# Kernel tuning notes

Hardware: AMD Instinct MI355X
Metric: run time of the kernel (lower is better)

Reference implementation:

```python
import jax, jax.numpy as jnp
import numpy as np
import math

EPS = 1e-5
MAX_NORM = 1.0 - 1e-3
C = 1.0
NUM_HEADS = 8


def _project(x, c=C):
    norm = jnp.maximum(jnp.linalg.norm(x, axis=-1, keepdims=True), EPS)
    max_norm = MAX_NORM / math.sqrt(c)
    return jnp.where(norm > max_norm, x / norm * max_norm, x)


def _expmap0(v, c=C):
    sc = math.sqrt(c)
    n = jnp.maximum(jnp.linalg.norm(v, axis=-1, keepdims=True), EPS)
    return _project(jnp.tanh(sc * n) * v / (sc * n), c)


def _logmap0(y, c=C):
    sc = math.sqrt(c)
    n = jnp.maximum(jnp.linalg.norm(y, axis=-1, keepdims=True), EPS)
    return jnp.arctanh(jnp.minimum(sc * n, 1.0 - EPS)) * y / (sc * n)


def _mobius_add(x, y, c=C):
    x2 = jnp.sum(x * x, axis=-1, keepdims=True)
    y2 = jnp.sum(y * y, axis=-1, keepdims=True)
    xy = jnp.sum(x * y, axis=-1, keepdims=True)
    num = (1.0 + 2.0 * c * xy + c * y2) * x + (1.0 - c * x2) * y
    den = jnp.maximum(1.0 + 2.0 * c * xy + c * c * x2 * y2, EPS)
    return _project(num / den, c)


def _pairwise_dist(x, y, c=C):
    # x: (B,H,Q,d), y: (B,H,K,d) -> (B,H,Q,K)
    m = _mobius_add(-x[:, :, :, None, :], y[:, :, None, :, :], c)  # (B,H,Q,K,d)
    n = jnp.clip(jnp.linalg.norm(m, axis=-1), EPS, 1.0 - EPS)
    sc = math.sqrt(c)
    return (2.0 / sc) * jnp.arctanh(sc * n)


def setup_inputs() -> dict:
    key = jax.random.key(0)
    ks = jax.random.split(key, 12)
    B, S, D = 2, 512, 512
    # points on the Poincare ball via expmap0
    q = _expmap0(0.5 * jax.random.normal(ks[0], (B, S, D), jnp.float32))
    k = _expmap0(0.5 * jax.random.normal(ks[1], (B, S, D), jnp.float32))
    v = _expmap0(0.5 * jax.random.normal(ks[2], (B, S, D), jnp.float32))
    w = 0.02
    return {
        'query': q, 'key': k, 'value': v,
        'Wq': w * jax.random.normal(ks[3], (D, D), jnp.float32),
        'bq': w * jax.random.normal(ks[4], (D,), jnp.float32),
        'Wk': w * jax.random.normal(ks[5], (D, D), jnp.float32),
        'bk': w * jax.random.normal(ks[6], (D,), jnp.float32),
        'Wv': w * jax.random.normal(ks[7], (D, D), jnp.float32),
        'bv': w * jax.random.normal(ks[8], (D,), jnp.float32),
        'Wo': w * jax.random.normal(ks[9], (D, D), jnp.float32),
        'bo': w * jax.random.normal(ks[10], (D,), jnp.float32),
    }


def reference(query, key, value, Wq, bq, Wk, bk, Wv, bv, Wo, bo):
    B, Q, D = query.shape
    K = key.shape[1]
    H = NUM_HEADS
    dh = D // H
    q_tan = _logmap0(query)
    k_tan = _logmap0(key)
    v_tan = _logmap0(value)
    q = (q_tan @ Wq.T + bq).reshape(B, Q, H, dh).transpose(0, 2, 1, 3)  # (B,H,Q,dh)
    k = (k_tan @ Wk.T + bk).reshape(B, K, H, dh).transpose(0, 2, 1, 3)
    v = (v_tan @ Wv.T + bv).reshape(B, K, H, dh).transpose(0, 2, 1, 3)
    q_hyp = _expmap0(q)
    k_hyp = _expmap0(k)
    scores = -_pairwise_dist(q_hyp, k_hyp) / math.sqrt(dh)  # (B,H,Q,K)
    attn = jax.nn.softmax(scores, axis=-1)  # dropout is identity in eval
    out = jnp.einsum('bhqk,bhkd->bhqd', attn, v)
    out = out.transpose(0, 2, 1, 3).reshape(B, Q, D)
    return _expmap0(out @ Wo.T + bo)
```

## Files before the change

### kernel.cpp

```cpp
#include <hip/hip_runtime.h>
#include <cmath>

#define DEV static __device__ __forceinline__

namespace {

constexpr int B = 2, S = 512, D = 512, H = 8;
constexpr int BS = B * S;
constexpr float EPSF = 1e-5f;
constexpr float MAXN = 1.0f - 1e-3f;
constexpr int NSPLIT = 4;

typedef unsigned short u16;
typedef unsigned int u32;
typedef __attribute__((ext_vector_type(8))) short bf8_t;
typedef __attribute__((ext_vector_type(8))) _Float16 h8_t;
typedef __attribute__((ext_vector_type(4))) float f4_t;

DEV float waveSum(float v) {
#pragma unroll
  for (int o = 32; o > 0; o >>= 1) v += __shfl_xor(v, o, 64);
  return v;
}
DEV u16 f2bf(float f) {
  u32 x = __float_as_uint(f);
  u32 r = x + 0x7fffu + ((x >> 16) & 1u);
  return (u16)(r >> 16);
}
DEV float bf2f(u16 u) { return __uint_as_float(((u32)u) << 16); }
DEV u16 f2h(float f) {
  _Float16 h = (_Float16)f;
  u16 u;
  __builtin_memcpy(&u, &h, 2);
  return u;
}
DEV float tanh_pos(float n) {
  float e = __builtin_amdgcn_exp2f(2.8853900817779268f * n);
  return (e - 1.f) / (e + 1.f);
}
DEV bf8_t conv8(float4 a, float4 b) {
  bf8_t o;
  o[0] = (short)f2bf(a.x); o[1] = (short)f2bf(a.y);
  o[2] = (short)f2bf(a.z); o[3] = (short)f2bf(a.w);
  o[4] = (short)f2bf(b.x); o[5] = (short)f2bf(b.y);
  o[6] = (short)f2bf(b.z); o[7] = (short)f2bf(b.w);
  return o;
}
DEV float dot4(float4 a) { return a.x * a.x + a.y * a.y + a.z * a.z + a.w * a.w; }

__global__ __launch_bounds__(256) void gemm_qkv_f2(
    const float* __restrict__ q, const float* __restrict__ k,
    const float* __restrict__ v, const float* __restrict__ Wq,
    const float* __restrict__ Wk, const float* __restrict__ Wv,
    const float* __restrict__ bq, const float* __restrict__ bk,
    const float* __restrict__ bv, u16* __restrict__ hq, u16* __restrict__ hk,
    u16* __restrict__ vT, float* __restrict__ qn2, float* __restrict__ kn2) {
  const int z = blockIdx.z;
  const float* A = z == 0 ? q : (z == 1 ? k : v);
  const float* W = z == 0 ? Wq : (z == 1 ? Wk : Wv);
  const float* bias = z == 0 ? bq : (z == 1 ? bk : bv);
  const int i0 = blockIdx.y * 64, j0 = blockIdx.x * 64, h = blockIdx.x;
  __shared__ __align__(16) u16 As[4096], Bs[4096];
  __shared__ float facs[64];
  const int tid = threadIdx.x;
  const int w = tid >> 6, l = tid & 63, lg = l >> 4, lr = l & 15;
  const int srow = tid >> 3, scb = tid & 7;
  f4_t acc[4] = {{0, 0, 0, 0}, {0, 0, 0, 0}, {0, 0, 0, 0}, {0, 0, 0, 0}};
  float n2a = 0.f, n2b = 0.f;
  for (int kt = 0; kt < D; kt += 64) {
    const float* ap0 = A + (size_t)(i0 + srow) * D + kt + scb * 8;
    const float* ap1 = ap0 + (size_t)32 * D;
    const float* wp0 = W + (size_t)(j0 + srow) * D + kt + scb * 8;
    const float* wp1 = wp0 + (size_t)32 * D;
    float4 a00 = *(const float4*)ap0, a01 = *(const float4*)(ap0 + 4);
    float4 a10 = *(const float4*)ap1, a11 = *(const float4*)(ap1 + 4);
    float4 w00 = *(const float4*)wp0, w01 = *(const float4*)(wp0 + 4);
    float4 w10 = *(const float4*)wp1, w11 = *(const float4*)(wp1 + 4);
    n2a += dot4(a00) + dot4(a01);
    n2b += dot4(a10) + dot4(a11);
    __syncthreads();
    const int sw = 8 * (scb ^ (srow & 7));
    *(bf8_t*)&As[srow * 64 + sw] = conv8(a00, a01);
    *(bf8_t*)&As[(srow + 32) * 64 + sw] = conv8(a10, a11);
    *(bf8_t*)&Bs[srow * 64 + sw] = conv8(w00, w01);
    *(bf8_t*)&Bs[(srow + 32) * 64 + sw] = conv8(w10, w11);
    __syncthreads();
#pragma unroll
    for (int ks = 0; ks < 2; ++ks) {
      const int arow = w * 16 + lr;
      bf8_t af = *(const bf8_t*)&As[arow * 64 + 8 * ((ks * 4 + lg) ^ (arow & 7))];
#pragma unroll
      for (int nf = 0; nf < 4; ++nf) {
        const int brow = nf * 16 + lr;
        bf8_t bfr = *(const bf8_t*)&Bs[brow * 64 + 8 * ((ks * 4 + lg) ^ (brow & 7))];
        acc[nf] = __builtin_amdgcn_mfma_f32_16x16x32_bf16(af, bfr, acc[nf], 0, 0, 0);
      }
    }
  }
  n2a += __shfl_xor(n2a, 1, 64); n2a += __shfl_xor(n2a, 2, 64);
  n2a += __shfl_xor(n2a, 4, 64);
  n2b += __shfl_xor(n2b, 1, 64); n2b += __shfl_xor(n2b, 2, 64);
  n2b += __shfl_xor(n2b, 4, 64);
  if (scb == 0) {
    float na = fmaxf(sqrtf(n2a), EPSF), za = fminf(na, 1.0f - EPSF);
    facs[srow] = 0.34657359027997264f *
                 __builtin_amdgcn_logf((1.0f + za) / (1.0f - za)) / na;
    float nb = fmaxf(sqrtf(n2b), EPSF), zb = fminf(nb, 1.0f - EPSF);
    facs[srow + 32] = 0.34657359027997264f *
                      __builtin_amdgcn_logf((1.0f + zb) / (1.0f - zb)) / nb;
  }
  __syncthreads();
  float c[4][4];
#pragma unroll
  for (int nf = 0; nf < 4; ++nf) {
    const float bb = bias[j0 + nf * 16 + lr];
#pragma unroll
    for (int r = 0; r < 4; ++r)
      c[nf][r] = acc[nf][r] * facs[w * 16 + lg * 4 + r] + bb;
  }
  if (z < 2) {
    float part[4] = {0, 0, 0, 0};
#pragma unroll
    for (int nf = 0; nf < 4; ++nf)
#pragma unroll
      for (int r = 0; r < 4; ++r) part[r] += c[nf][r] * c[nf][r];
#pragma unroll
    for (int off = 1; off < 16; off <<= 1)
#pragma unroll
      for (int r = 0; r < 4; ++r) part[r] += __shfl_xor(part[r], off, 64);
    float fac[4];
#pragma unroll
    for (int r = 0; r < 4; ++r) {
      float n = fmaxf(sqrtf(part[r]), EPSF);
      fac[r] = fminf(tanh_pos(n), MAXN) / n;
    }
    u16 yb[4][4];
    float p2[4] = {0, 0, 0, 0};
#pragma unroll
    for (int nf = 0; nf < 4; ++nf)
#pragma unroll
      for (int r = 0; r < 4; ++r) {
        u16 t = f2bf(c[nf][r] * fac[r]);
        yb[nf][r] = t;
        float yf = bf2f(t);
        p2[r] += yf * yf;
      }
#pragma unroll
    for (int off = 1; off < 16; off <<= 1)
#pragma unroll
      for (int r = 0; r < 4; ++r) p2[r] += __shfl_xor(p2[r], off, 64);
    u16* dst = z == 0 ? hq : hk;
    float* n2o = z == 0 ? qn2 : kn2;
#pragma unroll
    for (int nf = 0; nf < 4; ++nf)
#pragma unroll
      for (int r = 0; r < 4; ++r)
        dst[(size_t)(i0 + w * 16 + lg * 4 + r) * D + j0 + nf * 16 + lr] = yb[nf][r];
    if (lr == 0)
#pragma unroll
      for (int r = 0; r < 4; ++r)
        n2o[h * BS + i0 + w * 16 + lg * 4 + r] = p2[r];
  } else {
    __syncthreads();
#pragma unroll
    for (int nf = 0; nf < 4; ++nf)
#pragma unroll
      for (int r = 0; r < 4; ++r) {
        const int prow = w * 16 + lg * 4 + r;
        const int pcol = nf * 16 + lr;
        As[prow * 64 + 8 * ((pcol >> 3) ^ (prow & 7)) + (pcol & 7)] = f2h(c[nf][r]);
      }
    __syncthreads();
    const int d = tid >> 2, s0 = (tid & 3) * 16;
    const int b = i0 >> 9, sb = (i0 & 511) + s0;
    bf8_t o0, o1;
#pragma unroll
    for (int j = 0; j < 8; ++j) {
      const int s = s0 + j;
      o0[j] = (short)As[s * 64 + 8 * ((d >> 3) ^ (s & 7)) + (d & 7)];
    }
#pragma unroll
    for (int j = 0; j < 8; ++j) {
      const int s = s0 + 8 + j;
      o1[j] = (short)As[s * 64 + 8 * ((d >> 3) ^ (s & 7)) + (d & 7)];
    }
    u16* dst = vT + ((size_t)((b * 8 + h) * 64 + d)) * S + sb;
    *(bf8_t*)dst = o0;
    *(bf8_t*)(dst + 8) = o1;
  }
}

__global__ __launch_bounds__(64) void fused_attn_sk(
    const u16* __restrict__ hq, const u16* __restrict__ hk,
    const u16* __restrict__ vT, const float* __restrict__ qn2,
    const float* __restrict__ kn2, float* __restrict__ Opart,
    float* __restrict__ rpart) {
  const int bh = blockIdx.z, b = bh >> 3, h = bh & 7;
  const int i0 = blockIdx.x * 16;
  const int sp = blockIdx.y;
  __shared__ __align__(16) u16 Ps[2][16 * 64];
  const int l = threadIdx.x, lg = l >> 4, lr = l & 15;
  bf8_t qf[2];
#pragma unroll
  for (int ks = 0; ks < 2; ++ks)
    qf[ks] = *(const bf8_t*)(hq + (size_t)(b * S + i0 + lr) * D + h * 64 +
                             ks * 32 + lg * 8);
  float qq[4];
#pragma unroll
  for (int r = 0; r < 4; ++r) qq[r] = qn2[h * BS + b * S + i0 + lg * 4 + r];
  f4_t acc_o[4] = {{0, 0, 0, 0}, {0, 0, 0, 0}, {0, 0, 0, 0}, {0, 0, 0, 0}};
  float rsum[4] = {0, 0, 0, 0};
#pragma unroll
  for (int t = 0; t < 2; ++t) {
    const int kt = sp * 2 + t;
    const int kb = b * S + kt * 64;
    bf8_t kf[2][4], vf[2][4];
#pragma unroll
    for (int ks = 0; ks < 2; ++ks)
#pragma unroll
      for (int nf = 0; nf < 4; ++nf) {
        kf[ks][nf] = *(const bf8_t*)(hk + (size_t)(kb + nf * 16 + lr) * D +
                                     h * 64 + ks * 32 + lg * 8);
        vf[ks][nf] = *(const bf8_t*)(vT + (size_t)(bh * 64 + nf * 16 + lr) * S +
                                     kt * 64 + ks * 32 + lg * 8);
      }
    float kn[4];
#pragma unroll
    for (int nf = 0; nf < 4; ++nf) kn[nf] = kn2[h * BS + kb + nf * 16 + lr];
    f4_t sa[4] = {{0, 0, 0, 0}, {0, 0, 0, 0}, {0, 0, 0, 0}, {0, 0, 0, 0}};
#pragma unroll
    for (int ks = 0; ks < 2; ++ks)
#pragma unroll
      for (int nf = 0; nf < 4; ++nf)
        sa[nf] = __builtin_amdgcn_mfma_f32_16x16x32_bf16(qf[ks], kf[ks][nf],
                                                         sa[nf], 0, 0, 0);
    u16* Pb = Ps[t & 1];
    float ps[4] = {0, 0, 0, 0};
#pragma unroll
    for (int nf = 0; nf < 4; ++nf) {
      const float kk = kn[nf];
#pragma unroll
      for (int r = 0; r < 4; ++r) {
        const float tt = sa[nf][r];
        float num = fmaxf(qq[r] - 2.f * tt + kk, 0.f);
        float den = fmaxf(1.f - 2.f * tt + qq[r] * kk, EPSF);
        float rr = fminf(fmaxf(sqrtf(num / den), EPSF), MAXN);
        float p = __builtin_amdgcn_exp2f(
            0.125f * __builtin_amdgcn_logf((1.f - rr) / (1.f + rr)));
        ps[r] += p;
        const int prow = lg * 4 + r, pcol = nf * 16 + lr;
        Pb[prow * 64 + 8 * ((pcol >> 3) ^ (prow & 7)) + (pcol & 7)] = f2h(p);
      }
    }
#pragma unroll
    for (int off = 1; off < 16; off <<= 1)
#pragma unroll
      for (int r = 0; r < 4; ++r) ps[r] += __shfl_xor(ps[r], off, 64);
#pragma unroll
    for (int r = 0; r < 4; ++r) rsum[r] += ps[r];
#pragma unroll
    for (int ks = 0; ks < 2; ++ks) {
      h8_t pa = *(const h8_t*)&Pb[lr * 64 + 8 * ((ks * 4 + lg) ^ (lr & 7))];
#pragma unroll
      for (int nf = 0; nf < 4; ++nf)
        acc_o[nf] = __builtin_amdgcn_mfma_f32_16x16x32_f16(pa, vf[ks][nf],
                                                           acc_o[nf], 0, 0, 0);
    }
  }
  float* Ob = Opart + ((size_t)(sp * 16 + bh) * S + i0) * 64;
#pragma unroll
  for (int nf = 0; nf < 4; ++nf)
#pragma unroll
    for (int r = 0; r < 4; ++r)
      Ob[(lg * 4 + r) * 64 + nf * 16 + lr] = acc_o[nf][r];
  if (lr == 0)
#pragma unroll
    for (int r = 0; r < 4; ++r)
      rpart[(size_t)(sp * 16 + bh) * S + i0 + lg * 4 + r] = rsum[r];
}

__global__ __launch_bounds__(256) void combine_sk(
    const float* __restrict__ Opart, const float* __restrict__ rpart,
    u16* __restrict__ ctx) {
  const int e2 = blockIdx.x * 256 + threadIdx.x;
  const int idx = e2 * 2;
  const int bh = idx >> 15;
  const int rem = idx & 32767;
  const int qrow = rem >> 6, d = rem & 63;
  float rt = 0.f;
#pragma unroll
  for (int sp = 0; sp < NSPLIT; ++sp)
    rt += rpart[(size_t)(sp * 16 + bh) * S + qrow];
  float ox = 0.f, oy = 0.f;
#pragma unroll
  for (int sp = 0; sp < NSPLIT; ++sp) {
    float2 t = *(const float2*)&Opart[((size_t)(sp * 16 + bh) * S + qrow) * 64 + d];
    ox += t.x; oy += t.y;
  }
  float inv = 1.f / rt;
  ushort2 ov;
  ov.x = f2bf(ox * inv);
  ov.y = f2bf(oy * inv);
  const int token = (bh >> 3) * S + qrow, col = (bh & 7) * 64 + d;
  *(ushort2*)&ctx[(size_t)token * D + col] = ov;
}

__global__ __launch_bounds__(256) void gemm_out_f(
    const u16* __restrict__ A, const float* __restrict__ Wo,
    const float* __restrict__ bias, float* __restrict__ C) {
  const int i0 = blockIdx.y * 64, j0 = blockIdx.x * 64;
  __shared__ __align__(16) u16 As[4096], Bs[4096];
  const int tid = threadIdx.x;
  const int w = tid >> 6, l = tid & 63, lg = l >> 4, lr = l & 15;
  const int srow = tid >> 3, scb = tid & 7;
  f4_t acc[4] = {{0, 0, 0, 0}, {0, 0, 0, 0}, {0, 0, 0, 0}, {0, 0, 0, 0}};
  for (int kt = 0; kt < D; kt += 64) {
    bf8_t a0 = *(const bf8_t*)(A + (size_t)(i0 + srow) * D + kt + scb * 8);
    bf8_t a1 = *(const bf8_t*)(A + (size_t)(i0 + srow + 32) * D + kt + scb * 8);
    const float* wp0 = Wo + (size_t)(j0 + srow) * D + kt + scb * 8;
    const float* wp1 = wp0 + (size_t)32 * D;
    float4 w00 = *(const float4*)wp0, w01 = *(const float4*)(wp0 + 4);
    float4 w10 = *(const float4*)wp1, w11 = *(const float4*)(wp1 + 4);
    __syncthreads();
    const int sw = 8 * (scb ^ (srow & 7));
    *(bf8_t*)&As[srow * 64 + sw] = a0;
    *(bf8_t*)&As[(srow + 32) * 64 + sw] = a1;
    *(bf8_t*)&Bs[srow * 64 + sw] = conv8(w00, w01);
    *(bf8_t*)&Bs[(srow + 32) * 64 + sw] = conv8(w10, w11);
    __syncthreads();
#pragma unroll
    for (int ks = 0; ks < 2; ++ks) {
      const int arow = w * 16 + lr;
      bf8_t af = *(const bf8_t*)&As[arow * 64 + 8 * ((ks * 4 + lg) ^ (arow & 7))];
#pragma unroll
      for (int nf = 0; nf < 4; ++nf) {
        const int brow = nf * 16 + lr;
        bf8_t bfr = *(const bf8_t*)&Bs[brow * 64 + 8 * ((ks * 4 + lg) ^ (brow & 7))];
        acc[nf] = __builtin_amdgcn_mfma_f32_16x16x32_bf16(af, bfr, acc[nf], 0, 0, 0);
      }
    }
  }
#pragma unroll
  for (int nf = 0; nf < 4; ++nf) {
    const int j = j0 + nf * 16 + lr;
    const float bb = bias[j];
#pragma unroll
    for (int r = 0; r < 4; ++r)
      C[(size_t)(i0 + w * 16 + lg * 4 + r) * D + j] = acc[nf][r] + bb;
  }
}

__global__ __launch_bounds__(256) void expmap_rows_full(
    const float* __restrict__ in, float* __restrict__ out) {
  const int row = blockIdx.x;
  const float2 xv = *(const float2*)(in + (size_t)row * D + threadIdx.x * 2);
  float s = xv.x * xv.x + xv.y * xv.y;
  __shared__ float sh[4];
  float ws = waveSum(s);
  if ((threadIdx.x & 63) == 0) sh[threadIdx.x >> 6] = ws;
  __syncthreads();
  float tot = sh[0] + sh[1] + sh[2] + sh[3];
  float n = fmaxf(sqrtf(tot), EPSF);
  float fac = fminf(tanh_pos(n), MAXN) / n;
  float2 o = make_float2(xv.x * fac, xv.y * fac);
  *(float2*)(out + (size_t)row * D + threadIdx.x * 2) = o;
}

}

extern "C" void kernel_launch(void* const* d_in, const int* in_sizes, int n_in,
                              void* d_out, int out_size, void* d_ws,
                              size_t ws_size, hipStream_t stream) {
  const float* q = (const float*)d_in[0];
  const float* k = (const float*)d_in[1];
  const float* v = (const float*)d_in[2];
  const float* Wq = (const float*)d_in[3];
  const float* bq = (const float*)d_in[4];
  const float* Wk = (const float*)d_in[5];
  const float* bk = (const float*)d_in[6];
  const float* Wv = (const float*)d_in[7];
  const float* bv = (const float*)d_in[8];
  const float* Wo = (const float*)d_in[9];
  const float* bo = (const float*)d_in[10];
  float* out = (float*)d_out;

  char* w8 = (char*)d_ws;
  u16* hq = (u16*)(w8 + 0);
  u16* hk = (u16*)(w8 + 1048576);
  u16* vT = (u16*)(w8 + 2097152);
  float* qn2 = (float*)(w8 + 3145728);
  float* kn2 = (float*)(w8 + 3178496);
  u16* ctx = (u16*)(w8 + 3211264);
  float* olin = (float*)(w8 + 4259840);
  float* Opart = (float*)(w8 + 6291456);
  float* rpart = (float*)(w8 + 14680064);

  gemm_qkv_f2<<<dim3(8, 16, 3), 256, 0, stream>>>(q, k, v, Wq, Wk, Wv, bq, bk,
                                                  bv, hq, hk, vT, qn2, kn2);
  fused_attn_sk<<<dim3(32, NSPLIT, 16), 64, 0, stream>>>(hq, hk, vT, qn2, kn2,
                                                         Opart, rpart);
  combine_sk<<<dim3(1024), 256, 0, stream>>>(Opart, rpart, ctx);
  gemm_out_f<<<dim3(8, 16), 256, 0, stream>>>(ctx, Wo, bo, olin);
  expmap_rows_full<<<dim3(BS), 256, 0, stream>>>(olin, out);
}
```

Baseline: 46.19 us.

## Fuse split-K attention partial combine into attention block via shared memory

Each attention block now runs the four key splits as four waves of one 256-thread block. The partial outputs and row sums are reduced in shared memory, and ctx is written directly in bf16. This removes the separate combine kernel launch and the global round trip of the fp32 partial outputs (several MB). In exchange each block uses more LDS and needs a block barrier, and there are fewer, larger blocks.

```diff
diff --git a/kernel.cpp b/kernel.cpp
--- a/kernel.cpp
+++ b/kernel.cpp
@@ -9,7 +9,6 @@
 constexpr int BS = B * S;
 constexpr float EPSF = 1e-5f;
 constexpr float MAXN = 1.0f - 1e-3f;
-constexpr int NSPLIT = 4;
 
 typedef unsigned short u16;
 typedef unsigned int u32;
@@ -190,16 +189,17 @@
   }
 }
 
-__global__ __launch_bounds__(64) void fused_attn_sk(
+__global__ __launch_bounds__(256) void fused_attn_blk(
     const u16* __restrict__ hq, const u16* __restrict__ hk,
     const u16* __restrict__ vT, const float* __restrict__ qn2,
-    const float* __restrict__ kn2, float* __restrict__ Opart,
-    float* __restrict__ rpart) {
-  const int bh = blockIdx.z, b = bh >> 3, h = bh & 7;
+    const float* __restrict__ kn2, u16* __restrict__ ctx) {
+  const int bh = blockIdx.y, b = bh >> 3, h = bh & 7;
   const int i0 = blockIdx.x * 16;
-  const int sp = blockIdx.y;
-  __shared__ __align__(16) u16 Ps[2][16 * 64];
-  const int l = threadIdx.x, lg = l >> 4, lr = l & 15;
+  __shared__ __align__(16) u16 Ps[4][2][1024];
+  __shared__ float rsL[4][16];
+  const int tid = threadIdx.x;
+  const int w = tid >> 6, l = tid & 63, lg = l >> 4, lr = l & 15;
+  const int sp = w;
   bf8_t qf[2];
 #pragma unroll
   for (int ks = 0; ks < 2; ++ks)
@@ -209,7 +209,7 @@
 #pragma unroll
   for (int r = 0; r < 4; ++r) qq[r] = qn2[h * BS + b * S + i0 + lg * 4 + r];
   f4_t acc_o[4] = {{0, 0, 0, 0}, {0, 0, 0, 0}, {0, 0, 0, 0}, {0, 0, 0, 0}};
-  float rsum[4] = {0, 0, 0, 0};
+  float rloc[4] = {0, 0, 0, 0};
 #pragma unroll
   for (int t = 0; t < 2; ++t) {
     const int kt = sp * 2 + t;
@@ -234,7 +234,7 @@
       for (int nf = 0; nf < 4; ++nf)
         sa[nf] = __builtin_amdgcn_mfma_f32_16x16x32_bf16(qf[ks], kf[ks][nf],
                                                          sa[nf], 0, 0, 0);
-    u16* Pb = Ps[t & 1];
+    u16* Pb = Ps[w][t & 1];
     float ps[4] = {0, 0, 0, 0};
 #pragma unroll
     for (int nf = 0; nf < 4; ++nf) {
@@ -257,7 +257,7 @@
 #pragma unroll
       for (int r = 0; r < 4; ++r) ps[r] += __shfl_xor(ps[r], off, 64);
 #pragma unroll
-    for (int r = 0; r < 4; ++r) rsum[r] += ps[r];
+    for (int r = 0; r < 4; ++r) rloc[r] += ps[r];
 #pragma unroll
     for (int ks = 0; ks < 2; ++ks) {
       h8_t pa = *(const h8_t*)&Pb[lr * 64 + 8 * ((ks * 4 + lg) ^ (lr & 7))];
@@ -267,42 +267,28 @@
                                                            acc_o[nf], 0, 0, 0);
     }
   }
-  float* Ob = Opart + ((size_t)(sp * 16 + bh) * S + i0) * 64;
+  float* myO = (float*)Ps + w * 1024;
 #pragma unroll
   for (int nf = 0; nf < 4; ++nf)
 #pragma unroll
     for (int r = 0; r < 4; ++r)
-      Ob[(lg * 4 + r) * 64 + nf * 16 + lr] = acc_o[nf][r];
+      myO[(lg * 4 + r) * 64 + nf * 16 + lr] = acc_o[nf][r];
   if (lr == 0)
 #pragma unroll
-    for (int r = 0; r < 4; ++r)
-      rpart[(size_t)(sp * 16 + bh) * S + i0 + lg * 4 + r] = rsum[r];
-}
-
-__global__ __launch_bounds__(256) void combine_sk(
-    const float* __restrict__ Opart, const float* __restrict__ rpart,
-    u16* __restrict__ ctx) {
-  const int e2 = blockIdx.x * 256 + threadIdx.x;
-  const int idx = e2 * 2;
-  const int bh = idx >> 15;
-  const int rem = idx & 32767;
-  const int qrow = rem >> 6, d = rem & 63;
-  float rt = 0.f;
-#pragma unroll
-  for (int sp = 0; sp < NSPLIT; ++sp)
-    rt += rpart[(size_t)(sp * 16 + bh) * S + qrow];
-  float ox = 0.f, oy = 0.f;
-#pragma unroll
-  for (int sp = 0; sp < NSPLIT; ++sp) {
-    float2 t = *(const float2*)&Opart[((size_t)(sp * 16 + bh) * S + qrow) * 64 + d];
-    ox += t.x; oy += t.y;
-  }
-  float inv = 1.f / rt;
-  ushort2 ov;
-  ov.x = f2bf(ox * inv);
-  ov.y = f2bf(oy * inv);
-  const int token = (bh >> 3) * S + qrow, col = (bh & 7) * 64 + d;
-  *(ushort2*)&ctx[(size_t)token * D + col] = ov;
+    for (int r = 0; r < 4; ++r) rsL[w][lg * 4 + r] = rloc[r];
+  __syncthreads();
+  const float* OsL = (const float*)Ps;
+  const int row = tid >> 4, c4 = (tid & 15) * 4;
+  const float rt = rsL[0][row] + rsL[1][row] + rsL[2][row] + rsL[3][row];
+  const float inv = 1.f / rt;
+  f4_t s = {0, 0, 0, 0};
+#pragma unroll
+  for (int sp2 = 0; sp2 < 4; ++sp2)
+    s += *(const f4_t*)&OsL[sp2 * 1024 + row * 64 + c4];
+  ushort4 o;
+  o.x = f2bf(s[0] * inv); o.y = f2bf(s[1] * inv);
+  o.z = f2bf(s[2] * inv); o.w = f2bf(s[3] * inv);
+  *(ushort4*)&ctx[(size_t)(b * S + i0 + row) * D + h * 64 + c4] = o;
 }
 
 __global__ __launch_bounds__(256) void gemm_out_f(
@@ -392,14 +378,10 @@
   float* kn2 = (float*)(w8 + 3178496);
   u16* ctx = (u16*)(w8 + 3211264);
   float* olin = (float*)(w8 + 4259840);
-  float* Opart = (float*)(w8 + 6291456);
-  float* rpart = (float*)(w8 + 14680064);
 
   gemm_qkv_f2<<<dim3(8, 16, 3), 256, 0, stream>>>(q, k, v, Wq, Wk, Wv, bq, bk,
                                                   bv, hq, hk, vT, qn2, kn2);
-  fused_attn_sk<<<dim3(32, NSPLIT, 16), 64, 0, stream>>>(hq, hk, vT, qn2, kn2,
-                                                         Opart, rpart);
-  combine_sk<<<dim3(1024), 256, 0, stream>>>(Opart, rpart, ctx);
+  fused_attn_blk<<<dim3(32, 16), 256, 0, stream>>>(hq, hk, vT, qn2, kn2, ctx);
   gemm_out_f<<<dim3(8, 16), 256, 0, stream>>>(ctx, Wo, bo, olin);
   expmap_rows_full<<<dim3(BS), 256, 0, stream>>>(olin, out);
 }
```

Result: faster. 41.83 us (-9.5%).
